# Kernel optimization log

Measured on AMD Instinct MI355X. Metric: run time of the kernel, lower is better.

Reference implementation:

```python
import jax, jax.numpy as jnp
import numpy as np

# dims
B, T = 256, 64
N_AG, N_FEAT = 10, 4
X_DIM, X_PERM, X_STATIC = 44, 40, 10
HID, XEMB, NHID = 128, 32, 8
E = N_AG * (N_AG - 1)           # 90 directed edges (off-diagonal)
GEMB = NHID * E                 # 720 graph embedding per sample/step
RNN_IN = XEMB + 1 + GEMB        # 753
A_IN = X_STATIC + GEMB          # 730 (x_emb_size2==0 in GraphNN branch)
O_IN = XEMB + X_STATIC + 1 + GEMB  # 763

_off = np.ones((N_AG, N_AG)) - np.eye(N_AG)
RECV = jnp.asarray(np.where(_off)[0])  # rel_rec one-hot == gather by receiver idx
SEND = jnp.asarray(np.where(_off)[1])  # rel_send one-hot == gather by sender idx


def setup_inputs() -> dict:
    key = jax.random.key(0)
    ks = jax.random.split(key, 32)
    w = lambda k, shape: jax.random.normal(k, shape, jnp.float32) * 0.05
    return {
        'x': jax.random.normal(ks[0], (B, T + 1, X_DIM), jnp.float32),
        'x_demo': jax.random.normal(ks[1], (B, X_STATIC), jnp.float32),
        'f_treatment': jax.random.uniform(ks[2], (B, T + 1, 1), jnp.float32),
        'h0': jax.random.normal(ks[3], (B, HID), jnp.float32),
        # x2emb (Linear 4->32), x_static2emb (Linear 10->10)
        'W_x2emb': w(ks[4], (XEMB, X_DIM - X_PERM)), 'b_x2emb': w(ks[5], (XEMB,)),
        'W_stat': w(ks[6], (X_STATIC, X_STATIC)), 'b_stat': w(ks[7], (X_STATIC,)),
        # NRI-style MLP1 (node): 4->8->8 ; MLP2 (edge): 16->8->8
        'W_m1a': w(ks[8], (NHID, N_FEAT)), 'b_m1a': w(ks[9], (NHID,)),
        'W_m1b': w(ks[10], (NHID, NHID)), 'b_m1b': w(ks[11], (NHID,)),
        'W_m2a': w(ks[12], (NHID, 2 * NHID)), 'b_m2a': w(ks[13], (NHID,)),
        'W_m2b': w(ks[14], (NHID, NHID)), 'b_m2b': w(ks[15], (NHID,)),
        # treatment head: Linear(730->128)+ReLU, then Linear(128->1, no bias)
        'W_a1': w(ks[16], (HID, A_IN)), 'b_a1': w(ks[17], (HID,)),
        'W_a2': w(ks[18], (1, HID)),
        # outcome head: Linear(763->128)+ReLU, then Linear(128->1, no bias)
        'W_o1': w(ks[19], (HID, O_IN)), 'b_o1': w(ks[20], (HID,)),
        'W_o2': w(ks[21], (1, HID)),
        # GRUCell(753 -> 128)
        'W_ih': w(ks[22], (3 * HID, RNN_IN)), 'b_ih': w(ks[23], (3 * HID,)),
        'W_hh': w(ks[24], (3 * HID, HID)), 'b_hh': w(ks[25], (3 * HID,)),
    }


def reference(x, x_demo, f_treatment, h0, W_x2emb, b_x2emb, W_stat, b_stat,
              W_m1a, b_m1a, W_m1b, b_m1b, W_m2a, b_m2a, W_m2b, b_m2b,
              W_a1, b_a1, W_a2, W_o1, b_o1, W_o2, W_ih, b_ih, W_hh, b_hh):
    xt = x[:, :T]                       # (B,T,44); len_time = x.size(1)-1
    treat = f_treatment[:, :T]          # (B,T,1)
    demo = x_demo @ W_stat.T + b_stat   # (B,10) static embedding
    demoT = jnp.broadcast_to(demo[:, None], (B, T, X_STATIC))

    # --- GNN(x_permuted): mlp1 per node, node2edge gather, mlp2 per edge ---
    xa = xt[..., :X_PERM].reshape(B, T, N_AG, N_FEAT)
    h1 = jax.nn.elu(xa @ W_m1a.T + b_m1a)
    h1 = jax.nn.elu(h1 @ W_m1b.T + b_m1b)         # (B,T,N_AG,8); BN in eval = identity
    edges = jnp.concatenate([h1[:, :, RECV], h1[:, :, SEND]], axis=-1)  # (B,T,E,16)
    h2 = jax.nn.elu(edges @ W_m2a.T + b_m2a)
    h2 = jax.nn.elu(h2 @ W_m2b.T + b_m2b)         # (B,T,E,8)
    gemb = h2.reshape(B, T, GEMB)                 # (B,T,720)

    xemb = xt[..., X_PERM:] @ W_x2emb.T + b_x2emb  # (B,T,32)

    # --- treatment (a_or_ipw) head; dropout identity in eval ---
    a_in = jnp.concatenate([demoT, gemb], axis=-1)          # (B,T,730)
    a_out = jax.nn.relu(a_in @ W_a1.T + b_a1) @ W_a2.T      # (B,T,1)

    # --- outcome head ---
    o_in = jnp.concatenate([xemb, demoT, treat, gemb], axis=-1)  # (B,T,763)
    y_out = jax.nn.relu(o_in @ W_o1.T + b_o1) @ W_o2.T           # (B,T,1)

    # --- GRUCell recurrence over time ---
    rnn_in = jnp.concatenate([xemb, treat, gemb], axis=-1)  # (B,T,753)
    gi = rnn_in @ W_ih.T + b_ih                             # precompute input proj (B,T,3H)

    def step(h, g):
        gh = h @ W_hh.T + b_hh
        i_r, i_z, i_n = jnp.split(g, 3, axis=-1)
        h_r, h_z, h_n = jnp.split(gh, 3, axis=-1)
        r = jax.nn.sigmoid(i_r + h_r)
        z = jax.nn.sigmoid(i_z + h_z)
        n = jnp.tanh(i_n + r * h_n)
        h_new = (1.0 - z) * n + z * h
        return h_new, h_new

    _, hs = jax.lax.scan(step, h0, jnp.swapaxes(gi, 0, 1))
    hs = jnp.swapaxes(hs, 0, 1)                             # (B,T,128)

    return jnp.concatenate([a_out, y_out, hs], axis=-1)     # (B,T,130)
```

## Files before the change

### kernel.cpp

```cpp
#include <hip/hip_runtime.h>
#include <hip/hip_bf16.h>
#include <math.h>

#define BB     256
#define TT     64
#define BT     (BB*TT)
#define XD     44
#define XP     40
#define XS     10
#define HID    128
#define XEMB   32
#define NHID   8
#define NAG    10
#define NEDGE  90
#define GEMB   720
#define KF     768
#define NTOT   640

typedef __bf16  bf16_t;
typedef __bf16  bf16x8 __attribute__((ext_vector_type(8)));
typedef float   floatx4 __attribute__((ext_vector_type(4)));
typedef _Float16 half2_t __attribute__((ext_vector_type(2)));

__device__ __forceinline__ float elu_f(float v) { return v > 0.f ? v : expm1f(v); }
__device__ __forceinline__ float rcp_fast(float x) { return __builtin_amdgcn_rcpf(x); }
__device__ __forceinline__ float sigmoid_fast(float v) { return rcp_fast(1.f + __expf(-v)); }
__device__ __forceinline__ float tanh_fast(float x) { return 1.f - 2.f * rcp_fast(1.f + __expf(2.f * x)); }

__global__ __launch_bounds__(256) void prep_kernel(
    const float* __restrict__ Wa1, const float* __restrict__ ba1,
    const float* __restrict__ Wo1, const float* __restrict__ bo1,
    const float* __restrict__ Wih, const float* __restrict__ bih,
    bf16_t* __restrict__ WT, float* __restrict__ bcat) {
  int idx = blockIdx.x * 256 + threadIdx.x;
  if (idx >= NTOT * KF) return;
  int n = idx / KF, k = idx - n * KF;
  float v = 0.f;
  if (n < 128) {
    if (k >= 32 && k < 42)        v = Wa1[n * 730 + (k - 32)];
    else if (k >= 43 && k < 763)  v = Wa1[n * 730 + 10 + (k - 43)];
  } else if (n < 256) {
    int m = n - 128;
    if (k < 763)                  v = Wo1[m * 763 + k];
  } else {
    int m = n - 256;
    if (k < 32)                   v = Wih[m * 753 + k];
    else if (k == 42)             v = Wih[m * 753 + 32];
    else if (k >= 43 && k < 763)  v = Wih[m * 753 + 33 + (k - 43)];
  }
  WT[n * KF + k] = (bf16_t)v;
  if (k == 0) {
    bcat[n] = (n < 128) ? ba1[n] : (n < 256 ? bo1[n - 128] : bih[n - 256]);
  }
}

#define W_M1A 0
#define B_M1A 32
#define W_M1B 40
#define B_M1B 104
#define W_M2A 112
#define B_M2A 240
#define W_M2B 248
#define B_M2B 312
#define W_X2E 320
#define B_X2E 448
#define W_ST  480
#define B_ST  580
#define W_TOT 590
#define TOKS_PER_BLK 8

__global__ __launch_bounds__(64) void encoder_kernel(
    const float* __restrict__ x, const float* __restrict__ x_demo,
    const float* __restrict__ ftreat,
    const float* __restrict__ Wm1a, const float* __restrict__ bm1a,
    const float* __restrict__ Wm1b, const float* __restrict__ bm1b,
    const float* __restrict__ Wm2a, const float* __restrict__ bm2a,
    const float* __restrict__ Wm2b, const float* __restrict__ bm2b,
    const float* __restrict__ Wx2e, const float* __restrict__ bx2e,
    const float* __restrict__ Wst, const float* __restrict__ bst,
    bf16_t* __restrict__ F) {
  int blk = blockIdx.x;
  int b = blk >> 3, tc = blk & 7;
  int tid = threadIdx.x;

  __shared__ float w[W_TOT];
  __shared__ float demoL[XS];
  __shared__ float xl[XD];
  __shared__ float h1a[NAG * 8];
  __shared__ float h1s[NAG * 8];
  __shared__ float h2a[NEDGE * 8];

  for (int i = tid; i < 32;  i += 64) w[W_M1A + i] = Wm1a[i];
  for (int i = tid; i < 8;   i += 64) w[B_M1A + i] = bm1a[i];
  for (int i = tid; i < 64;  i += 64) w[W_M1B + i] = Wm1b[i];
  for (int i = tid; i < 8;   i += 64) w[B_M1B + i] = bm1b[i];
  for (int i = tid; i < 128; i += 64) w[W_M2A + i] = Wm2a[i];
  for (int i = tid; i < 8;   i += 64) w[B_M2A + i] = bm2a[i];
  for (int i = tid; i < 64;  i += 64) w[W_M2B + i] = Wm2b[i];
  for (int i = tid; i < 8;   i += 64) w[B_M2B + i] = bm2b[i];
  for (int i = tid; i < 128; i += 64) w[W_X2E + i] = Wx2e[i];
  for (int i = tid; i < 32;  i += 64) w[B_X2E + i] = bx2e[i];
  for (int i = tid; i < 100; i += 64) w[W_ST + i]  = Wst[i];
  for (int i = tid; i < 10;  i += 64) w[B_ST + i]  = bst[i];
  __syncthreads();

  if (tid < 10) {
    float s = w[B_ST + tid];
#pragma unroll
    for (int j = 0; j < 10; j++) s += x_demo[b * XS + j] * w[W_ST + tid * 10 + j];
    demoL[tid] = s;
  }
  __syncthreads();

  for (int ti = 0; ti < TOKS_PER_BLK; ti++) {
    int t = tc * TOKS_PER_BLK + ti;
    int tok = b * TT + t;
    if (tid < XD) xl[tid] = x[(size_t)(b * 65 + t) * XD + tid];
    __syncthreads();

    for (int c = tid; c < NAG * 8; c += 64) {
      int i = c >> 3, o = c & 7;
      float s = w[B_M1A + o];
#pragma unroll
      for (int f = 0; f < 4; f++) s += xl[i * 4 + f] * w[W_M1A + o * 4 + f];
      h1a[c] = elu_f(s);
    }
    __syncthreads();
    for (int c = tid; c < NAG * 8; c += 64) {
      int i = c >> 3, o = c & 7;
      float s = w[B_M1B + o];
#pragma unroll
      for (int p = 0; p < 8; p++) s += h1a[i * 8 + p] * w[W_M1B + o * 8 + p];
      h1s[c] = elu_f(s);
    }
    __syncthreads();
    for (int c = tid; c < NEDGE * 8; c += 64) {
      int e = c >> 3, o = c & 7;
      int r = e / 9, q = e - 9 * r;
      int sd = q + (q >= r ? 1 : 0);
      float s = w[B_M2A + o];
#pragma unroll
      for (int kk = 0; kk < 8; kk++) s += h1s[r * 8 + kk]  * w[W_M2A + o * 16 + kk];
#pragma unroll
      for (int kk = 0; kk < 8; kk++) s += h1s[sd * 8 + kk] * w[W_M2A + o * 16 + 8 + kk];
      h2a[c] = elu_f(s);
    }
    __syncthreads();

    bf16_t* Frow = F + (size_t)tok * KF;
    for (int c = tid; c < NEDGE * 8; c += 64) {
      int e = c >> 3, o = c & 7;
      float s = w[B_M2B + o];
#pragma unroll
      for (int kk = 0; kk < 8; kk++) s += h2a[e * 8 + kk] * w[W_M2B + o * 8 + kk];
      Frow[43 + c] = (bf16_t)elu_f(s);
    }
    if (tid < 32) {
      float s = w[B_X2E + tid];
#pragma unroll
      for (int f = 0; f < 4; f++) s += xl[40 + f] * w[W_X2E + tid * 4 + f];
      Frow[tid] = (bf16_t)s;
    } else if (tid < 42) {
      Frow[tid] = (bf16_t)demoL[tid - 32];
    } else if (tid == 42) {
      Frow[42] = (bf16_t)ftreat[b * 65 + t];
    } else if (tid < 48) {
      Frow[720 + tid] = (bf16_t)0.f;
    }
    __syncthreads();
  }
}

__global__ __launch_bounds__(256) void gemm_kernel(
    const bf16_t* __restrict__ F, const bf16_t* __restrict__ WT,
    const float* __restrict__ bcat, float* __restrict__ G) {
  __shared__ __align__(16) bf16_t As[128 * 32];
  __shared__ __align__(16) bf16_t Bs[128 * 32];

  int tid  = threadIdx.x;
  int lane = tid & 63;
  int wv   = tid >> 6;
  int wr   = wv >> 1, wc = wv & 1;
  int m0 = blockIdx.x * 128, n0 = blockIdx.y * 128;

  floatx4 acc[4][4];
#pragma unroll
  for (int i = 0; i < 4; i++)
#pragma unroll
    for (int j = 0; j < 4; j++) acc[i][j] = floatx4{0.f, 0.f, 0.f, 0.f};

  int c0 = tid, c1 = tid + 256;
  int r0 = c0 >> 2, p0 = c0 & 3;
  int r1 = c1 >> 2, p1 = c1 & 3;
  int qr = lane >> 4;
  int lr = lane & 15;

  for (int k0 = 0; k0 < KF; k0 += 32) {
    uint4 a0 = *(const uint4*)(F  + (size_t)(m0 + r0) * KF + k0 + p0 * 8);
    uint4 a1 = *(const uint4*)(F  + (size_t)(m0 + r1) * KF + k0 + p1 * 8);
    uint4 b0 = *(const uint4*)(WT + (size_t)(n0 + r0) * KF + k0 + p0 * 8);
    uint4 b1 = *(const uint4*)(WT + (size_t)(n0 + r1) * KF + k0 + p1 * 8);
    __syncthreads();
    ((uint4*)As)[c0] = a0; ((uint4*)As)[c1] = a1;
    ((uint4*)Bs)[c0] = b0; ((uint4*)Bs)[c1] = b1;
    __syncthreads();

    bf16x8 af[4], bf[4];
#pragma unroll
    for (int i = 0; i < 4; i++) {
      af[i] = *(const bf16x8*)(As + (wr * 64 + i * 16 + lr) * 32 + qr * 8);
      bf[i] = *(const bf16x8*)(Bs + (wc * 64 + i * 16 + lr) * 32 + qr * 8);
    }
#pragma unroll
    for (int i = 0; i < 4; i++)
#pragma unroll
      for (int j = 0; j < 4; j++)
        acc[i][j] = __builtin_amdgcn_mfma_f32_16x16x32_bf16(af[i], bf[j], acc[i][j], 0, 0, 0);
  }

#pragma unroll
  for (int i = 0; i < 4; i++) {
#pragma unroll
    for (int j = 0; j < 4; j++) {
      int col = n0 + wc * 64 + j * 16 + lr;
      float bv = bcat[col];
#pragma unroll
      for (int r = 0; r < 4; r++) {
        int row = m0 + wr * 64 + i * 16 + qr * 4 + r;
        G[(size_t)row * NTOT + col] = acc[i][j][r] + bv;
      }
    }
  }
}

__global__ __launch_bounds__(256) void head_kernel(
    const float* __restrict__ G, const float* __restrict__ Wa2,
    const float* __restrict__ Wo2, float* __restrict__ out) {
  int wid  = (blockIdx.x * 256 + threadIdx.x) >> 6;
  int lane = threadIdx.x & 63;
  const float* g = G + (size_t)wid * NTOT;
  float sa = fmaxf(g[lane], 0.f) * Wa2[lane] + fmaxf(g[lane + 64], 0.f) * Wa2[lane + 64];
  float sy = fmaxf(g[128 + lane], 0.f) * Wo2[lane] + fmaxf(g[192 + lane], 0.f) * Wo2[lane + 64];
#pragma unroll
  for (int off = 32; off > 0; off >>= 1) {
    sa += __shfl_down(sa, off, 64);
    sy += __shfl_down(sy, off, 64);
  }
  if (lane == 0) {
    out[(size_t)wid * 130 + 0] = sa;
    out[(size_t)wid * 130 + 1] = sy;
  }
}

__global__ __launch_bounds__(128, 2) void gru_kernel(
    const float* __restrict__ G, const float* __restrict__ h0,
    const float* __restrict__ Whh, const float* __restrict__ bhh,
    float* __restrict__ out) {
  int b = blockIdx.x;
  int tid = threadIdx.x;
  int lane = tid & 63;

  __shared__ unsigned int h2[2][HID / 2];

  const float* gbase = G + (size_t)b * TT * NTOT;

  half2_t wr[64], wz[64], wn[64];
#pragma unroll
  for (int l = 0; l < 64; l++) {
    float2 a = *(const float2*)(Whh + (size_t)tid * HID + 2 * l);
    wr[l] = half2_t{(_Float16)a.x, (_Float16)a.y};
  }
#pragma unroll
  for (int l = 0; l < 64; l++) {
    float2 a = *(const float2*)(Whh + (size_t)(HID + tid) * HID + 2 * l);
    wz[l] = half2_t{(_Float16)a.x, (_Float16)a.y};
  }
#pragma unroll
  for (int l = 0; l < 64; l++) {
    float2 a = *(const float2*)(Whh + (size_t)(2 * HID + tid) * HID + 2 * l);
    wn[l] = half2_t{(_Float16)a.x, (_Float16)a.y};
  }
  float br = bhh[tid], bz = bhh[HID + tid], bn = bhh[2 * HID + tid];

  float hprev = h0[(size_t)b * HID + tid];
  ((_Float16*)h2[0])[tid] = (_Float16)hprev;
  float ir = gbase[256 + tid], iz = gbase[384 + tid], inn = gbase[512 + tid];
  __syncthreads();

  for (int t = 0; t < TT; t++) {
    unsigned int hl = h2[t & 1][lane];
    float nir = 0.f, niz = 0.f, ninn = 0.f;
    if (t + 1 < TT) {
      const float* gn = gbase + (size_t)(t + 1) * NTOT;
      nir  = gn[256 + tid];
      niz  = gn[384 + tid];
      ninn = gn[512 + tid];
    }
    float sr0 = 0.f, sr1 = 0.f, sz0 = 0.f, sz1 = 0.f, sn0 = 0.f, sn1 = 0.f;
#pragma unroll
    for (int l = 0; l < 64; l += 2) {
      int p0 = __builtin_amdgcn_readlane((int)hl, l);
      int p1 = __builtin_amdgcn_readlane((int)hl, l + 1);
      half2_t q0 = __builtin_bit_cast(half2_t, p0);
      half2_t q1 = __builtin_bit_cast(half2_t, p1);
      sr0 = __builtin_amdgcn_fdot2(wr[l],     q0, sr0, false);
      sr1 = __builtin_amdgcn_fdot2(wr[l + 1], q1, sr1, false);
      sz0 = __builtin_amdgcn_fdot2(wz[l],     q0, sz0, false);
      sz1 = __builtin_amdgcn_fdot2(wz[l + 1], q1, sz1, false);
      sn0 = __builtin_amdgcn_fdot2(wn[l],     q0, sn0, false);
      sn1 = __builtin_amdgcn_fdot2(wn[l + 1], q1, sn1, false);
    }
    float r  = sigmoid_fast(ir + sr0 + sr1 + br);
    float z  = sigmoid_fast(iz + sz0 + sz1 + bz);
    float nn = tanh_fast(inn + r * (sn0 + sn1 + bn));
    float hn = (1.f - z) * nn + z * hprev;
    hprev = hn;
    ((_Float16*)h2[(t + 1) & 1])[tid] = (_Float16)hn;
    __syncthreads();
    out[(size_t)(b * TT + t) * 130 + 2 + tid] = hn;
    ir = nir; iz = niz; inn = ninn;
  }
}

extern "C" void kernel_launch(void* const* d_in, const int* in_sizes, int n_in,
                              void* d_out, int out_size, void* d_ws, size_t ws_size,
                              hipStream_t stream) {
  const float* x      = (const float*)d_in[0];
  const float* x_demo = (const float*)d_in[1];
  const float* ftr    = (const float*)d_in[2];
  const float* h0     = (const float*)d_in[3];
  const float* Wx2e   = (const float*)d_in[4];
  const float* bx2e   = (const float*)d_in[5];
  const float* Wst    = (const float*)d_in[6];
  const float* bst    = (const float*)d_in[7];
  const float* Wm1a   = (const float*)d_in[8];
  const float* bm1a   = (const float*)d_in[9];
  const float* Wm1b   = (const float*)d_in[10];
  const float* bm1b   = (const float*)d_in[11];
  const float* Wm2a   = (const float*)d_in[12];
  const float* bm2a   = (const float*)d_in[13];
  const float* Wm2b   = (const float*)d_in[14];
  const float* bm2b   = (const float*)d_in[15];
  const float* Wa1    = (const float*)d_in[16];
  const float* ba1    = (const float*)d_in[17];
  const float* Wa2    = (const float*)d_in[18];
  const float* Wo1    = (const float*)d_in[19];
  const float* bo1    = (const float*)d_in[20];
  const float* Wo2    = (const float*)d_in[21];
  const float* Wih    = (const float*)d_in[22];
  const float* bih    = (const float*)d_in[23];
  const float* Whh    = (const float*)d_in[24];
  const float* bhh    = (const float*)d_in[25];
  float* out = (float*)d_out;

  char* ws = (char*)d_ws;
  bf16_t* F   = (bf16_t*)(ws);
  bf16_t* WT  = (bf16_t*)(ws + 25165824);
  float*  bc  = (float*)(ws + 25165824 + 983040);
  float*  G   = (float*)(ws + 25165824 + 983040 + 2560);

  prep_kernel<<<dim3((NTOT * KF + 255) / 256), dim3(256), 0, stream>>>(
      Wa1, ba1, Wo1, bo1, Wih, bih, WT, bc);
  encoder_kernel<<<dim3(BT / TOKS_PER_BLK), dim3(64), 0, stream>>>(
      x, x_demo, ftr, Wm1a, bm1a, Wm1b, bm1b, Wm2a, bm2a, Wm2b, bm2b,
      Wx2e, bx2e, Wst, bst, F);
  gemm_kernel<<<dim3(BT / 128, NTOT / 128), dim3(256), 0, stream>>>(F, WT, bc, G);
  head_kernel<<<dim3(BT / 4), dim3(256), 0, stream>>>(G, Wa2, Wo2, out);
  gru_kernel<<<dim3(BB), dim3(128), 0, stream>>>(G, h0, Whh, bhh, out);
}
```

Measured before the change: 262.5 us.

## Restructure encoder: per-edge threads, fp16 dot2, aligned 16-byte F row stores

Rewrites the graph encoder so each lane computes a full node or a full edge (all 8 outputs) in registers with fp16 packed dot2 instructions, instead of per-output scalar loops separated by several barriers. The F feature layout is shifted so the edge embedding starts at column 48, which allows 16-byte vector stores, and the prep kernel's weight transpose is updated to match. Token count per block is halved and the block count doubled, giving more parallelism. Using fp16 for intermediate activations and weights, plus a fast exp-based ELU, lowers precision in exchange for throughput.

```diff
diff --git a/kernel.cpp b/kernel.cpp
--- a/kernel.cpp
+++ b/kernel.cpp
@@ -17,15 +17,28 @@
 #define KF     768
 #define NTOT   640
 
+
 typedef __bf16  bf16_t;
 typedef __bf16  bf16x8 __attribute__((ext_vector_type(8)));
 typedef float   floatx4 __attribute__((ext_vector_type(4)));
 typedef _Float16 half2_t __attribute__((ext_vector_type(2)));
-
-__device__ __forceinline__ float elu_f(float v) { return v > 0.f ? v : expm1f(v); }
+typedef _Float16 half4_t __attribute__((ext_vector_type(4)));
+typedef _Float16 half8_t __attribute__((ext_vector_type(8)));
+
 __device__ __forceinline__ float rcp_fast(float x) { return __builtin_amdgcn_rcpf(x); }
 __device__ __forceinline__ float sigmoid_fast(float v) { return rcp_fast(1.f + __expf(-v)); }
 __device__ __forceinline__ float tanh_fast(float x) { return 1.f - 2.f * rcp_fast(1.f + __expf(2.f * x)); }
+__device__ __forceinline__ float elu_fast(float v) { return v > 0.f ? v : __expf(v) - 1.f; }
+__device__ __forceinline__ float fdot2f(half2_t a, half2_t b, float acc) {
+  return __builtin_amdgcn_fdot2(a, b, acc, false);
+}
+__device__ __forceinline__ float dot8h(half8_t a, half8_t b, float acc) {
+  acc = fdot2f(half2_t{a[0], a[1]}, half2_t{b[0], b[1]}, acc);
+  acc = fdot2f(half2_t{a[2], a[3]}, half2_t{b[2], b[3]}, acc);
+  acc = fdot2f(half2_t{a[4], a[5]}, half2_t{b[4], b[5]}, acc);
+  acc = fdot2f(half2_t{a[6], a[7]}, half2_t{b[6], b[7]}, acc);
+  return acc;
+}
 
 __global__ __launch_bounds__(256) void prep_kernel(
     const float* __restrict__ Wa1, const float* __restrict__ ba1,
@@ -37,37 +50,23 @@
   int n = idx / KF, k = idx - n * KF;
   float v = 0.f;
   if (n < 128) {
-    if (k >= 32 && k < 42)        v = Wa1[n * 730 + (k - 32)];
-    else if (k >= 43 && k < 763)  v = Wa1[n * 730 + 10 + (k - 43)];
+    if (k >= 32 && k < 42)  v = Wa1[n * 730 + (k - 32)];
+    else if (k >= 48)       v = Wa1[n * 730 + 10 + (k - 48)];
   } else if (n < 256) {
     int m = n - 128;
-    if (k < 763)                  v = Wo1[m * 763 + k];
+    if (k < 43)             v = Wo1[m * 763 + k];
+    else if (k >= 48)       v = Wo1[m * 763 + 43 + (k - 48)];
   } else {
     int m = n - 256;
-    if (k < 32)                   v = Wih[m * 753 + k];
-    else if (k == 42)             v = Wih[m * 753 + 32];
-    else if (k >= 43 && k < 763)  v = Wih[m * 753 + 33 + (k - 43)];
+    if (k < 32)             v = Wih[m * 753 + k];
+    else if (k == 42)       v = Wih[m * 753 + 32];
+    else if (k >= 48)       v = Wih[m * 753 + 33 + (k - 48)];
   }
   WT[n * KF + k] = (bf16_t)v;
   if (k == 0) {
     bcat[n] = (n < 128) ? ba1[n] : (n < 256 ? bo1[n - 128] : bih[n - 256]);
   }
 }
-
-#define W_M1A 0
-#define B_M1A 32
-#define W_M1B 40
-#define B_M1B 104
-#define W_M2A 112
-#define B_M2A 240
-#define W_M2B 248
-#define B_M2B 312
-#define W_X2E 320
-#define B_X2E 448
-#define W_ST  480
-#define B_ST  580
-#define W_TOT 590
-#define TOKS_PER_BLK 8
 
 __global__ __launch_bounds__(64) void encoder_kernel(
     const float* __restrict__ x, const float* __restrict__ x_demo,
@@ -80,92 +79,150 @@
     const float* __restrict__ Wst, const float* __restrict__ bst,
     bf16_t* __restrict__ F) {
   int blk = blockIdx.x;
-  int b = blk >> 3, tc = blk & 7;
-  int tid = threadIdx.x;
-
-  __shared__ float w[W_TOT];
+  int b = blk >> 4, tc = blk & 15;
+  int lane = threadIdx.x;
+
+  __shared__ __align__(16) _Float16 h1sp[NAG * 8];
+  __shared__ __align__(16) _Float16 w2aR[64];
+  __shared__ __align__(16) _Float16 w2aS[64];
+  __shared__ __align__(16) _Float16 w2bp[64];
   __shared__ float demoL[XS];
-  __shared__ float xl[XD];
-  __shared__ float h1a[NAG * 8];
-  __shared__ float h1s[NAG * 8];
-  __shared__ float h2a[NEDGE * 8];
-
-  for (int i = tid; i < 32;  i += 64) w[W_M1A + i] = Wm1a[i];
-  for (int i = tid; i < 8;   i += 64) w[B_M1A + i] = bm1a[i];
-  for (int i = tid; i < 64;  i += 64) w[W_M1B + i] = Wm1b[i];
-  for (int i = tid; i < 8;   i += 64) w[B_M1B + i] = bm1b[i];
-  for (int i = tid; i < 128; i += 64) w[W_M2A + i] = Wm2a[i];
-  for (int i = tid; i < 8;   i += 64) w[B_M2A + i] = bm2a[i];
-  for (int i = tid; i < 64;  i += 64) w[W_M2B + i] = Wm2b[i];
-  for (int i = tid; i < 8;   i += 64) w[B_M2B + i] = bm2b[i];
-  for (int i = tid; i < 128; i += 64) w[W_X2E + i] = Wx2e[i];
-  for (int i = tid; i < 32;  i += 64) w[B_X2E + i] = bx2e[i];
-  for (int i = tid; i < 100; i += 64) w[W_ST + i]  = Wst[i];
-  for (int i = tid; i < 10;  i += 64) w[B_ST + i]  = bst[i];
+
+  if (lane < 8) {
+    float4 v0 = *(const float4*)(Wm2a + lane * 16);
+    float4 v1 = *(const float4*)(Wm2a + lane * 16 + 4);
+    float4 v2 = *(const float4*)(Wm2a + lane * 16 + 8);
+    float4 v3 = *(const float4*)(Wm2a + lane * 16 + 12);
+    *(half8_t*)&w2aR[lane * 8] = half8_t{
+        (_Float16)v0.x, (_Float16)v0.y, (_Float16)v0.z, (_Float16)v0.w,
+        (_Float16)v1.x, (_Float16)v1.y, (_Float16)v1.z, (_Float16)v1.w};
+    *(half8_t*)&w2aS[lane * 8] = half8_t{
+        (_Float16)v2.x, (_Float16)v2.y, (_Float16)v2.z, (_Float16)v2.w,
+        (_Float16)v3.x, (_Float16)v3.y, (_Float16)v3.z, (_Float16)v3.w};
+    float4 u0 = *(const float4*)(Wm2b + lane * 8);
+    float4 u1 = *(const float4*)(Wm2b + lane * 8 + 4);
+    *(half8_t*)&w2bp[lane * 8] = half8_t{
+        (_Float16)u0.x, (_Float16)u0.y, (_Float16)u0.z, (_Float16)u0.w,
+        (_Float16)u1.x, (_Float16)u1.y, (_Float16)u1.z, (_Float16)u1.w};
+  }
+  if (lane < 10) {
+    float s = bst[lane];
+#pragma unroll
+    for (int j = 0; j < 10; j++) s += x_demo[b * XS + j] * Wst[lane * 10 + j];
+    demoL[lane] = s;
+  }
+
+  half4_t wA[8]; float bA[8];
+  half8_t wB1[8]; float bB1[8];
+  float bR[8], bG[8];
+#pragma unroll
+  for (int o = 0; o < 8; o++) {
+    float4 v = *(const float4*)(Wm1a + o * 4);
+    wA[o] = half4_t{(_Float16)v.x, (_Float16)v.y, (_Float16)v.z, (_Float16)v.w};
+    bA[o] = bm1a[o];
+    float4 w0 = *(const float4*)(Wm1b + o * 8);
+    float4 w1 = *(const float4*)(Wm1b + o * 8 + 4);
+    wB1[o] = half8_t{(_Float16)w0.x, (_Float16)w0.y, (_Float16)w0.z, (_Float16)w0.w,
+                     (_Float16)w1.x, (_Float16)w1.y, (_Float16)w1.z, (_Float16)w1.w};
+    bB1[o] = bm1b[o];
+    bR[o] = bm2a[o];
+    bG[o] = bm2b[o];
+  }
+  half4_t wX; float bX;
+  {
+    float4 v = *(const float4*)(Wx2e + (lane & 31) * 4);
+    wX = half4_t{(_Float16)v.x, (_Float16)v.y, (_Float16)v.z, (_Float16)v.w};
+    bX = bx2e[lane & 31];
+  }
   __syncthreads();
-
-  if (tid < 10) {
-    float s = w[B_ST + tid];
-#pragma unroll
-    for (int j = 0; j < 10; j++) s += x_demo[b * XS + j] * w[W_ST + tid * 10 + j];
-    demoL[tid] = s;
-  }
-  __syncthreads();
-
-  for (int ti = 0; ti < TOKS_PER_BLK; ti++) {
-    int t = tc * TOKS_PER_BLK + ti;
+  float demov = (lane >= 32 && lane < 42) ? demoL[lane - 32] : 0.f;
+
+  for (int ti = 0; ti < 4; ti++) {
+    int t = tc * 4 + ti;
     int tok = b * TT + t;
-    if (tid < XD) xl[tid] = x[(size_t)(b * 65 + t) * XD + tid];
+    const float* row = x + (size_t)(b * 65 + t) * XD;
+    bf16_t* Frow = F + (size_t)tok * KF;
+
+    if (lane < NAG) {
+      float4 xa = *(const float4*)(row + lane * 4);
+      half2_t x0{(_Float16)xa.x, (_Float16)xa.y};
+      half2_t x1{(_Float16)xa.z, (_Float16)xa.w};
+      float h1v[8];
+#pragma unroll
+      for (int o = 0; o < 8; o++) {
+        float s = bA[o];
+        s = fdot2f(x0, half2_t{wA[o][0], wA[o][1]}, s);
+        s = fdot2f(x1, half2_t{wA[o][2], wA[o][3]}, s);
+        h1v[o] = elu_fast(s);
+      }
+      half2_t e0{(_Float16)h1v[0], (_Float16)h1v[1]};
+      half2_t e1{(_Float16)h1v[2], (_Float16)h1v[3]};
+      half2_t e2{(_Float16)h1v[4], (_Float16)h1v[5]};
+      half2_t e3{(_Float16)h1v[6], (_Float16)h1v[7]};
+      half8_t hout;
+#pragma unroll
+      for (int o = 0; o < 8; o++) {
+        float s = bB1[o];
+        s = fdot2f(e0, half2_t{wB1[o][0], wB1[o][1]}, s);
+        s = fdot2f(e1, half2_t{wB1[o][2], wB1[o][3]}, s);
+        s = fdot2f(e2, half2_t{wB1[o][4], wB1[o][5]}, s);
+        s = fdot2f(e3, half2_t{wB1[o][6], wB1[o][7]}, s);
+        hout[o] = (_Float16)elu_fast(s);
+      }
+      *(half8_t*)&h1sp[lane * 8] = hout;
+    }
     __syncthreads();
 
-    for (int c = tid; c < NAG * 8; c += 64) {
-      int i = c >> 3, o = c & 7;
-      float s = w[B_M1A + o];
-#pragma unroll
-      for (int f = 0; f < 4; f++) s += xl[i * 4 + f] * w[W_M1A + o * 4 + f];
-      h1a[c] = elu_f(s);
-    }
-    __syncthreads();
-    for (int c = tid; c < NAG * 8; c += 64) {
-      int i = c >> 3, o = c & 7;
-      float s = w[B_M1B + o];
-#pragma unroll
-      for (int p = 0; p < 8; p++) s += h1a[i * 8 + p] * w[W_M1B + o * 8 + p];
-      h1s[c] = elu_f(s);
-    }
-    __syncthreads();
-    for (int c = tid; c < NEDGE * 8; c += 64) {
-      int e = c >> 3, o = c & 7;
-      int r = e / 9, q = e - 9 * r;
-      int sd = q + (q >= r ? 1 : 0);
-      float s = w[B_M2A + o];
-#pragma unroll
-      for (int kk = 0; kk < 8; kk++) s += h1s[r * 8 + kk]  * w[W_M2A + o * 16 + kk];
-#pragma unroll
-      for (int kk = 0; kk < 8; kk++) s += h1s[sd * 8 + kk] * w[W_M2A + o * 16 + 8 + kk];
-      h2a[c] = elu_f(s);
-    }
-    __syncthreads();
-
-    bf16_t* Frow = F + (size_t)tok * KF;
-    for (int c = tid; c < NEDGE * 8; c += 64) {
-      int e = c >> 3, o = c & 7;
-      float s = w[B_M2B + o];
-#pragma unroll
-      for (int kk = 0; kk < 8; kk++) s += h2a[e * 8 + kk] * w[W_M2B + o * 8 + kk];
-      Frow[43 + c] = (bf16_t)elu_f(s);
-    }
-    if (tid < 32) {
-      float s = w[B_X2E + tid];
-#pragma unroll
-      for (int f = 0; f < 4; f++) s += xl[40 + f] * w[W_X2E + tid * 4 + f];
-      Frow[tid] = (bf16_t)s;
-    } else if (tid < 42) {
-      Frow[tid] = (bf16_t)demoL[tid - 32];
-    } else if (tid == 42) {
+#pragma unroll
+    for (int q = 0; q < 2; q++) {
+      int e = lane + 64 * q;
+      if (e < NEDGE) {
+        int r = (e * 57) >> 9;
+        int sd = e - 9 * r;
+        sd += (sd >= r) ? 1 : 0;
+        half8_t hr = *(const half8_t*)&h1sp[r * 8];
+        half8_t hs = *(const half8_t*)&h1sp[sd * 8];
+        float av[8];
+#pragma unroll
+        for (int o = 0; o < 8; o++) {
+          half8_t wr8 = *(const half8_t*)&w2aR[o * 8];
+          half8_t ws8 = *(const half8_t*)&w2aS[o * 8];
+          float s = bR[o];
+          s = dot8h(hr, wr8, s);
+          s = dot8h(hs, ws8, s);
+          av[o] = elu_fast(s);
+        }
+        half2_t a0{(_Float16)av[0], (_Float16)av[1]};
+        half2_t a1{(_Float16)av[2], (_Float16)av[3]};
+        half2_t a2{(_Float16)av[4], (_Float16)av[5]};
+        half2_t a3{(_Float16)av[6], (_Float16)av[7]};
+        union { bf16_t h[8]; uint4 u; } pk;
+#pragma unroll
+        for (int o = 0; o < 8; o++) {
+          half8_t wb8 = *(const half8_t*)&w2bp[o * 8];
+          float s = bG[o];
+          s = fdot2f(a0, half2_t{wb8[0], wb8[1]}, s);
+          s = fdot2f(a1, half2_t{wb8[2], wb8[3]}, s);
+          s = fdot2f(a2, half2_t{wb8[4], wb8[5]}, s);
+          s = fdot2f(a3, half2_t{wb8[6], wb8[7]}, s);
+          pk.h[o] = (bf16_t)elu_fast(s);
+        }
+        *(uint4*)(Frow + 48 + e * 8) = pk.u;
+      }
+    }
+
+    float4 xe = *(const float4*)(row + XP);
+    if (lane < 32) {
+      float s = bX;
+      s = fdot2f(half2_t{(_Float16)xe.x, (_Float16)xe.y}, half2_t{wX[0], wX[1]}, s);
+      s = fdot2f(half2_t{(_Float16)xe.z, (_Float16)xe.w}, half2_t{wX[2], wX[3]}, s);
+      Frow[lane] = (bf16_t)s;
+    } else if (lane < 42) {
+      Frow[lane] = (bf16_t)demov;
+    } else if (lane == 42) {
       Frow[42] = (bf16_t)ftreat[b * 65 + t];
-    } else if (tid < 48) {
-      Frow[720 + tid] = (bf16_t)0.f;
+    } else if (lane < 48) {
+      Frow[lane] = (bf16_t)0.f;
     }
     __syncthreads();
   }
@@ -361,7 +418,7 @@
 
   prep_kernel<<<dim3((NTOT * KF + 255) / 256), dim3(256), 0, stream>>>(
       Wa1, ba1, Wo1, bo1, Wih, bih, WT, bc);
-  encoder_kernel<<<dim3(BT / TOKS_PER_BLK), dim3(64), 0, stream>>>(
+  encoder_kernel<<<dim3(BB * 16), dim3(64), 0, stream>>>(
       x, x_demo, ftr, Wm1a, bm1a, Wm1b, bm1b, Wm2a, bm2a, Wm2b, bm2b,
       Wx2e, bx2e, Wst, bst, F);
   gemm_kernel<<<dim3(BT / 128, NTOT / 128), dim3(256), 0, stream>>>(F, WT, bc, G);
```

Result: faster. 227.5 us (-13.3%).
